# Performance work log

Measured on AMD Instinct MI355X. Metric: run time of the kernel, lower is better.

The kernel has to match this reference:

```python
import jax, jax.numpy as jnp
import numpy as np

B, A = 65536, 32          # batch, n_agents
D, H1, H2, L = 4, 32, 32, 16  # local MLP dims
G_IN, G_H, G_OUT = 2 * L, 32, 2  # global MLP dims


def _lin_init(k, fan_in, fan_out):
    kw, kb = jax.random.split(k)
    s = 1.0 / np.sqrt(fan_in)
    W = jax.random.uniform(kw, (fan_in, fan_out), minval=-s, maxval=s, dtype=jnp.float32)
    b = jax.random.uniform(kb, (fan_out,), minval=-s, maxval=s, dtype=jnp.float32)
    return W, b


def setup_inputs() -> dict:
    key = jax.random.key(0)
    ks = jax.random.split(key, 9)
    x = jax.random.uniform(ks[0], (B, A * D), dtype=jnp.float32)
    oW1, ob1 = _lin_init(ks[1], D, H1)
    oW2, ob2 = _lin_init(ks[2], H1, H2)
    oW3, ob3 = _lin_init(ks[3], H2, L)
    sW1, sb1 = _lin_init(ks[4], D, H1)
    sW2, sb2 = _lin_init(ks[5], H1, H2)
    sW3, sb3 = _lin_init(ks[6], H2, L)
    gW1, gb1 = _lin_init(ks[7], G_IN, G_H)
    gW2, gb2 = _lin_init(ks[8], G_H, G_OUT)
    return {
        "joint_state_actions": x,
        "selected_agent_idx": 5,
        "oW1": oW1, "ob1": ob1, "oW2": oW2, "ob2": ob2, "oW3": oW3, "ob3": ob3,
        "sW1": sW1, "sb1": sb1, "sW2": sW2, "sb2": sb2, "sW3": sW3, "sb3": sb3,
        "gW1": gW1, "gb1": gb1, "gW2": gW2, "gb2": gb2,
    }


def _mlp3(x, W1, b1, W2, b2, W3, b3):
    h = jax.nn.relu(x @ W1 + b1)
    h = jax.nn.relu(h @ W2 + b2)
    return jax.nn.relu(h @ W3 + b3)


def reference(joint_state_actions, selected_agent_idx,
              oW1, ob1, oW2, ob2, oW3, ob3,
              sW1, sb1, sW2, sb2, sW3, sb3,
              gW1, gb1, gW2, gb2):
    xa = joint_state_actions.reshape(-1, A, D)  # [B, A, 4]
    # other-agents stack applied to all agents at once, masked sum over non-selected
    other = _mlp3(xa, oW1, ob1, oW2, ob2, oW3, ob3)  # [B, A, 16]
    mask = (jnp.arange(A) != selected_agent_idx).astype(other.dtype)[None, :, None]
    sum_other = jnp.sum(other * mask, axis=1)  # [B, 16]
    sel_in = xa[:, selected_agent_idx]  # [B, 4] (static index)
    sel_out = _mlp3(sel_in, sW1, sb1, sW2, sb2, sW3, sb3)  # [B, 16]
    h = jax.nn.relu(jnp.concatenate([sel_out, sum_other], axis=1) @ gW1 + gb1)
    q = h @ gW2 + gb2  # [B, 2]
    actions = sel_in[:, 3].astype(jnp.int32)[:, None]  # [B, 1]
    return jnp.take_along_axis(q, actions, axis=1)  # [B, 1]
```

## Files before the change

kernel.cpp:

```cpp
#include <hip/hip_runtime.h>
#include <hip/hip_bf16.h>

#define DEV __device__ __forceinline__

typedef __attribute__((ext_vector_type(8)))  __bf16    bf16x8;
typedef __attribute__((ext_vector_type(4)))  int       int4v;
typedef __attribute__((ext_vector_type(2)))  unsigned  uint2v;
typedef __attribute__((ext_vector_type(16))) float     vfloat16;

#if __has_builtin(__builtin_amdgcn_permlane32_swap)
#define HAVE_PLSWAP 1
#endif

DEV int pkbf(float a, float b) {
    unsigned ua = __builtin_bit_cast(unsigned, a) + 0x8000u;
    unsigned ub = __builtin_bit_cast(unsigned, b) + 0x8000u;
    return (int)__builtin_amdgcn_perm(ua, ub, 0x03020706u);
}

DEV bf16x8 i4_to_frag(int4v v) { return __builtin_bit_cast(bf16x8, v); }

DEV vfloat16 mfma32(bf16x8 a, bf16x8 b, vfloat16 c) {
    return __builtin_amdgcn_mfma_f32_32x32x16_bf16(a, b, c, 0, 0, 0);
}

DEV bf16x8 xposeB(float c0, float c1, float c2, float c3,
                  float c4, float c5, float c6, float c7, bool h) {
    int R0 = pkbf(fmaxf(c0, 0.f), fmaxf(c1, 0.f));
    int R1 = pkbf(fmaxf(c2, 0.f), fmaxf(c3, 0.f));
    int R2 = pkbf(fmaxf(c4, 0.f), fmaxf(c5, 0.f));
    int R3 = pkbf(fmaxf(c6, 0.f), fmaxf(c7, 0.f));
#ifdef HAVE_PLSWAP
    uint2v p0 = __builtin_amdgcn_permlane32_swap((unsigned)R0, (unsigned)R2, false, false);
    uint2v p1 = __builtin_amdgcn_permlane32_swap((unsigned)R1, (unsigned)R3, false, false);
    int4v v;
    v.x = (int)p0.x; v.y = (int)p1.x; v.z = (int)p0.y; v.w = (int)p1.y;
#else
    int S0 = h ? R0 : R2;
    int S1 = h ? R1 : R3;
    int Y0 = __shfl_xor(S0, 32, 64);
    int Y1 = __shfl_xor(S1, 32, 64);
    int4v v;
    v.x = h ? Y0 : R0;
    v.y = h ? Y1 : R1;
    v.z = h ? R2 : Y0;
    v.w = h ? R3 : Y1;
#endif
    return i4_to_frag(v);
}

DEV bf16x8 make_afrag(const float* __restrict__ W, const float* __restrict__ bias,
                      int ld, int Mact, int K, int koff, int lane) {
    int m = lane & 31;
    int h = lane >> 5;
    int d[4];
#pragma unroll
    for (int i = 0; i < 4; ++i) {
        int k0 = koff + h * 8 + 2 * i;
        int k1 = k0 + 1;
        float w0 = 0.f, w1 = 0.f;
        if (m < Mact) {
            if (k0 < K) w0 = W[k0 * ld + m];
            else if (bias && k0 == K) w0 = bias[m];
            if (k1 < K) w1 = W[k1 * ld + m];
            else if (bias && k1 == K) w1 = bias[m];
        }
        d[i] = pkbf(w0, w1);
    }
    int4v v; v.x = d[0]; v.y = d[1]; v.z = d[2]; v.w = d[3];
    return i4_to_frag(v);
}

DEV vfloat16 bvec32(const float* __restrict__ b, int lane) {
    int h = lane >> 5;
    vfloat16 v;
#pragma unroll
    for (int reg = 0; reg < 16; ++reg)
        v[reg] = b[(reg & 3) + 8 * (reg >> 2) + 4 * h];
    return v;
}
DEV vfloat16 bvec16(const float* __restrict__ b, int lane) {
    int h = lane >> 5;
    vfloat16 v;
#pragma unroll
    for (int reg = 0; reg < 16; ++reg)
        v[reg] = (reg < 8) ? b[(reg & 3) + 8 * (reg >> 2) + 4 * h] : 0.f;
    return v;
}

DEV vfloat16 zero16() {
    vfloat16 z;
#pragma unroll
    for (int i = 0; i < 16; ++i) z[i] = 0.f;
    return z;
}

DEV bf16x8 b1_from(int2 d) {
    int4v v;
    v.x = d.x;
    v.y = d.y;
    v.z = 0x00003f80;
    v.w = 0;
    return i4_to_frag(v);
}

struct Frags {
    bf16x8 A1, A2lo, A2hi, A3lo, A3hi;
    vfloat16 b2, b3;
};

DEV void load_frags(Frags& F,
                    const float* __restrict__ W1, const float* __restrict__ b1,
                    const float* __restrict__ W2, const float* __restrict__ b2,
                    const float* __restrict__ W3, const float* __restrict__ b3,
                    int lane) {
    F.A1   = make_afrag(W1, b1,      32, 32, 4,  0,  lane);
    F.A2lo = make_afrag(W2, nullptr, 32, 32, 32, 0,  lane);
    F.A2hi = make_afrag(W2, nullptr, 32, 32, 32, 16, lane);
    F.A3lo = make_afrag(W3, nullptr, 16, 16, 32, 0,  lane);
    F.A3hi = make_afrag(W3, nullptr, 16, 16, 32, 16, lane);
    F.b2 = bvec32(b2, lane);
    F.b3 = bvec16(b3, lane);
}

DEV vfloat16 run_mlp3(bf16x8 B1, const Frags& F, bool h) {
    vfloat16 C1 = mfma32(F.A1, B1, zero16());
    bf16x8 Blo = xposeB(C1[0], C1[1], C1[2], C1[3], C1[4], C1[5], C1[6], C1[7], h);
    bf16x8 Bhi = xposeB(C1[8], C1[9], C1[10], C1[11], C1[12], C1[13], C1[14], C1[15], h);
    vfloat16 C2 = mfma32(F.A2lo, Blo, F.b2);
    C2 = mfma32(F.A2hi, Bhi, C2);
    Blo = xposeB(C2[0], C2[1], C2[2], C2[3], C2[4], C2[5], C2[6], C2[7], h);
    Bhi = xposeB(C2[8], C2[9], C2[10], C2[11], C2[12], C2[13], C2[14], C2[15], h);
    vfloat16 C3 = mfma32(F.A3lo, Blo, F.b3);
    C3 = mfma32(F.A3hi, Bhi, C3);
    return C3;
}

#define XSTRIDE 66

__global__ __launch_bounds__(256)
void dqn_kernel(const float* __restrict__ x, const int* __restrict__ selp,
                const float* __restrict__ oW1, const float* __restrict__ ob1,
                const float* __restrict__ oW2, const float* __restrict__ ob2,
                const float* __restrict__ oW3, const float* __restrict__ ob3,
                const float* __restrict__ sW1, const float* __restrict__ sb1,
                const float* __restrict__ sW2, const float* __restrict__ sb2,
                const float* __restrict__ sW3, const float* __restrict__ sb3,
                const float* __restrict__ gW1, const float* __restrict__ gb1,
                const float* __restrict__ gW2, const float* __restrict__ gb2,
                float* __restrict__ out)
{
    __shared__ int   lds_xb[32 * XSTRIDE];
    __shared__ float lds_red[3][8][64];

    const int tid  = threadIdx.x;
    const int lane = tid & 63;
    const int wave = tid >> 6;
    const bool h = lane >= 32;
    const int c = lane & 31;
    const int sel = *selp;
    const int base0 = blockIdx.x * 32;

    {
        const float* xblk = x + (size_t)base0 * 128;
#pragma unroll
        for (int k = 0; k < 4; ++k) {
            int f = tid + 256 * k;
            int row = f >> 5;
            int ag  = f & 31;
            float4 v = *(const float4*)(xblk + (size_t)f * 4);
            int2 d;
            d.x = pkbf(v.x, v.y);
            d.y = pkbf(v.z, v.w);
            *(int2*)&lds_xb[ag * XSTRIDE + row * 2] = d;
        }
    }

    Frags Fo;
    load_frags(Fo, oW1, ob1, oW2, ob2, oW3, ob3, lane);

    __syncthreads();

    float sum[8] = {0.f, 0.f, 0.f, 0.f, 0.f, 0.f, 0.f, 0.f};
    const int a0 = wave * 8;
    const int* xb = &lds_xb[a0 * XSTRIDE + c * 2];

#pragma unroll
    for (int i = 0; i < 8; i += 2) {
        int2 da = *(const int2*)(xb + i * XSTRIDE);
        int2 db = *(const int2*)(xb + (i + 1) * XSTRIDE);

        vfloat16 C1a = mfma32(Fo.A1, b1_from(da), zero16());
        vfloat16 C1b = mfma32(Fo.A1, b1_from(db), zero16());

        bf16x8 Bal = xposeB(C1a[0], C1a[1], C1a[2], C1a[3], C1a[4], C1a[5], C1a[6], C1a[7], h);
        bf16x8 Bbl = xposeB(C1b[0], C1b[1], C1b[2], C1b[3], C1b[4], C1b[5], C1b[6], C1b[7], h);
        bf16x8 Bah = xposeB(C1a[8], C1a[9], C1a[10], C1a[11], C1a[12], C1a[13], C1a[14], C1a[15], h);
        bf16x8 Bbh = xposeB(C1b[8], C1b[9], C1b[10], C1b[11], C1b[12], C1b[13], C1b[14], C1b[15], h);

        vfloat16 C2a = mfma32(Fo.A2lo, Bal, Fo.b2);
        vfloat16 C2b = mfma32(Fo.A2lo, Bbl, Fo.b2);
        C2a = mfma32(Fo.A2hi, Bah, C2a);
        C2b = mfma32(Fo.A2hi, Bbh, C2b);

        Bal = xposeB(C2a[0], C2a[1], C2a[2], C2a[3], C2a[4], C2a[5], C2a[6], C2a[7], h);
        Bbl = xposeB(C2b[0], C2b[1], C2b[2], C2b[3], C2b[4], C2b[5], C2b[6], C2b[7], h);
        Bah = xposeB(C2a[8], C2a[9], C2a[10], C2a[11], C2a[12], C2a[13], C2a[14], C2a[15], h);
        Bbh = xposeB(C2b[8], C2b[9], C2b[10], C2b[11], C2b[12], C2b[13], C2b[14], C2b[15], h);

        vfloat16 C3a = mfma32(Fo.A3lo, Bal, Fo.b3);
        vfloat16 C3b = mfma32(Fo.A3lo, Bbl, Fo.b3);
        C3a = mfma32(Fo.A3hi, Bah, C3a);
        C3b = mfma32(Fo.A3hi, Bbh, C3b);

        if (a0 + i != sel) {
#pragma unroll
            for (int j = 0; j < 8; ++j) sum[j] += fmaxf(C3a[j], 0.f);
        }
        if (a0 + i + 1 != sel) {
#pragma unroll
            for (int j = 0; j < 8; ++j) sum[j] += fmaxf(C3b[j], 0.f);
        }
    }

    if (wave != 0) {
#pragma unroll
        for (int i = 0; i < 8; ++i) lds_red[wave - 1][i][lane] = sum[i];
    }
    __syncthreads();

    if (wave == 0) {
#pragma unroll
        for (int j = 0; j < 3; ++j)
#pragma unroll
            for (int i = 0; i < 8; ++i) sum[i] += lds_red[j][i][lane];

        Frags Fs;
        load_frags(Fs, sW1, sb1, sW2, sb2, sW3, sb3, lane);
        int2 ds = *(const int2*)&lds_xb[sel * XSTRIDE + c * 2];
        vfloat16 C3s = run_mlp3(b1_from(ds), Fs, h);

        bf16x8 Ag_lo = make_afrag(gW1, nullptr, 32, 32, 32, 0,  lane);
        bf16x8 Ag_hi = make_afrag(gW1, nullptr, 32, 32, 32, 16, lane);
        vfloat16 gb1v = bvec32(gb1, lane);
        bf16x8 Bg_lo = xposeB(C3s[0], C3s[1], C3s[2], C3s[3],
                              C3s[4], C3s[5], C3s[6], C3s[7], h);
        bf16x8 Bg_hi = xposeB(sum[0], sum[1], sum[2], sum[3],
                              sum[4], sum[5], sum[6], sum[7], h);
        vfloat16 G = mfma32(Ag_lo, Bg_lo, gb1v);
        G = mfma32(Ag_hi, Bg_hi, G);
#pragma unroll
        for (int i = 0; i < 16; ++i) G[i] = fmaxf(G[i], 0.f);

        float q0 = 0.f, q1 = 0.f;
#pragma unroll
        for (int reg = 0; reg < 16; ++reg) {
            int row = (reg & 3) + 8 * (reg >> 2) + (h ? 4 : 0);
            q0 += G[reg] * gW2[row * 2 + 0];
            q1 += G[reg] * gW2[row * 2 + 1];
        }
        q0 += __shfl_xor(q0, 32, 64);
        q1 += __shfl_xor(q1, 32, 64);
        q0 += gb2[0];
        q1 += gb2[1];

        if (!h) {
            float f3 = x[(size_t)(base0 + c) * 128 + sel * 4 + 3];
            int act = (int)f3;
            act = act < 0 ? 0 : (act > 1 ? 1 : act);
            out[base0 + c] = act ? q1 : q0;
        }
    }
}

extern "C" void kernel_launch(void* const* d_in, const int* in_sizes, int n_in,
                              void* d_out, int out_size, void* d_ws, size_t ws_size,
                              hipStream_t stream) {
    const float* x   = (const float*)d_in[0];
    const int*   sel = (const int*)d_in[1];
    const float* oW1 = (const float*)d_in[2];
    const float* ob1 = (const float*)d_in[3];
    const float* oW2 = (const float*)d_in[4];
    const float* ob2 = (const float*)d_in[5];
    const float* oW3 = (const float*)d_in[6];
    const float* ob3 = (const float*)d_in[7];
    const float* sW1 = (const float*)d_in[8];
    const float* sb1 = (const float*)d_in[9];
    const float* sW2 = (const float*)d_in[10];
    const float* sb2 = (const float*)d_in[11];
    const float* sW3 = (const float*)d_in[12];
    const float* sb3 = (const float*)d_in[13];
    const float* gW1 = (const float*)d_in[14];
    const float* gb1 = (const float*)d_in[15];
    const float* gW2 = (const float*)d_in[16];
    const float* gb2 = (const float*)d_in[17];
    float* out = (float*)d_out;

    const int B = in_sizes[0] / 128;
    const int blocks = B / 32;
    dqn_kernel<<<blocks, 256, 0, stream>>>(x, sel,
                                           oW1, ob1, oW2, ob2, oW3, ob3,
                                           sW1, sb1, sW2, sb2, sW3, sb3,
                                           gW1, gb1, gW2, gb2, out);
}
```

Measured before the change: 135.2 us.

## Process two batch tiles per block with double-buffered LDS prefetch

Each block now handles two 32-row tiles and uses a double-buffered LDS staging area. Waves 1-3 load and convert the next tile while wave 0 runs the selected-agent and global MLP tail for the current tile. The agent loop processes one agent per iteration instead of two interleaved, adds the layer-3 bias after the MFMA, and pins occupancy with a waves_per_eu attribute. The aim is to hide the serial wave-0 tail and the global-load latency, at the cost of less MFMA interleaving, weights being re-read every tile, and half as many blocks.

```diff
diff --git a/kernel.cpp b/kernel.cpp
--- a/kernel.cpp
+++ b/kernel.cpp
@@ -22,6 +22,13 @@
 
 DEV vfloat16 mfma32(bf16x8 a, bf16x8 b, vfloat16 c) {
     return __builtin_amdgcn_mfma_f32_32x32x16_bf16(a, b, c, 0, 0, 0);
+}
+
+DEV vfloat16 zc() {
+    vfloat16 z;
+#pragma unroll
+    for (int i = 0; i < 16; ++i) z[i] = 0.f;
+    return z;
 }
 
 DEV bf16x8 xposeB(float c0, float c1, float c2, float c3,
@@ -79,21 +86,6 @@
         v[reg] = b[(reg & 3) + 8 * (reg >> 2) + 4 * h];
     return v;
 }
-DEV vfloat16 bvec16(const float* __restrict__ b, int lane) {
-    int h = lane >> 5;
-    vfloat16 v;
-#pragma unroll
-    for (int reg = 0; reg < 16; ++reg)
-        v[reg] = (reg < 8) ? b[(reg & 3) + 8 * (reg >> 2) + 4 * h] : 0.f;
-    return v;
-}
-
-DEV vfloat16 zero16() {
-    vfloat16 z;
-#pragma unroll
-    for (int i = 0; i < 16; ++i) z[i] = 0.f;
-    return z;
-}
 
 DEV bf16x8 b1_from(int2 d) {
     int4v v;
@@ -104,41 +96,11 @@
     return i4_to_frag(v);
 }
 
-struct Frags {
-    bf16x8 A1, A2lo, A2hi, A3lo, A3hi;
-    vfloat16 b2, b3;
-};
-
-DEV void load_frags(Frags& F,
-                    const float* __restrict__ W1, const float* __restrict__ b1,
-                    const float* __restrict__ W2, const float* __restrict__ b2,
-                    const float* __restrict__ W3, const float* __restrict__ b3,
-                    int lane) {
-    F.A1   = make_afrag(W1, b1,      32, 32, 4,  0,  lane);
-    F.A2lo = make_afrag(W2, nullptr, 32, 32, 32, 0,  lane);
-    F.A2hi = make_afrag(W2, nullptr, 32, 32, 32, 16, lane);
-    F.A3lo = make_afrag(W3, nullptr, 16, 16, 32, 0,  lane);
-    F.A3hi = make_afrag(W3, nullptr, 16, 16, 32, 16, lane);
-    F.b2 = bvec32(b2, lane);
-    F.b3 = bvec16(b3, lane);
-}
-
-DEV vfloat16 run_mlp3(bf16x8 B1, const Frags& F, bool h) {
-    vfloat16 C1 = mfma32(F.A1, B1, zero16());
-    bf16x8 Blo = xposeB(C1[0], C1[1], C1[2], C1[3], C1[4], C1[5], C1[6], C1[7], h);
-    bf16x8 Bhi = xposeB(C1[8], C1[9], C1[10], C1[11], C1[12], C1[13], C1[14], C1[15], h);
-    vfloat16 C2 = mfma32(F.A2lo, Blo, F.b2);
-    C2 = mfma32(F.A2hi, Bhi, C2);
-    Blo = xposeB(C2[0], C2[1], C2[2], C2[3], C2[4], C2[5], C2[6], C2[7], h);
-    Bhi = xposeB(C2[8], C2[9], C2[10], C2[11], C2[12], C2[13], C2[14], C2[15], h);
-    vfloat16 C3 = mfma32(F.A3lo, Blo, F.b3);
-    C3 = mfma32(F.A3hi, Bhi, C3);
-    return C3;
-}
-
 #define XSTRIDE 66
+#define TILES_PER_BLK 2
 
 __global__ __launch_bounds__(256)
+__attribute__((amdgpu_waves_per_eu(4, 4)))
 void dqn_kernel(const float* __restrict__ x, const int* __restrict__ selp,
                 const float* __restrict__ oW1, const float* __restrict__ ob1,
                 const float* __restrict__ oW2, const float* __restrict__ ob2,
@@ -150,7 +112,7 @@
                 const float* __restrict__ gW2, const float* __restrict__ gb2,
                 float* __restrict__ out)
 {
-    __shared__ int   lds_xb[32 * XSTRIDE];
+    __shared__ int   lds_xb[2][32 * XSTRIDE];
     __shared__ float lds_red[3][8][64];
 
     const int tid  = threadIdx.x;
@@ -159,10 +121,10 @@
     const bool h = lane >= 32;
     const int c = lane & 31;
     const int sel = *selp;
-    const int base0 = blockIdx.x * 32;
 
     {
-        const float* xblk = x + (size_t)base0 * 128;
+        int tile0 = blockIdx.x * TILES_PER_BLK;
+        const float* xblk = x + (size_t)tile0 * 32 * 128;
 #pragma unroll
         for (int k = 0; k < 4; ++k) {
             int f = tid + 256 * k;
@@ -172,103 +134,127 @@
             int2 d;
             d.x = pkbf(v.x, v.y);
             d.y = pkbf(v.z, v.w);
-            *(int2*)&lds_xb[ag * XSTRIDE + row * 2] = d;
+            *(int2*)&lds_xb[0][ag * XSTRIDE + row * 2] = d;
         }
     }
 
-    Frags Fo;
-    load_frags(Fo, oW1, ob1, oW2, ob2, oW3, ob3, lane);
-
-    __syncthreads();
-
-    float sum[8] = {0.f, 0.f, 0.f, 0.f, 0.f, 0.f, 0.f, 0.f};
-    const int a0 = wave * 8;
-    const int* xb = &lds_xb[a0 * XSTRIDE + c * 2];
-
-#pragma unroll
-    for (int i = 0; i < 8; i += 2) {
-        int2 da = *(const int2*)(xb + i * XSTRIDE);
-        int2 db = *(const int2*)(xb + (i + 1) * XSTRIDE);
-
-        vfloat16 C1a = mfma32(Fo.A1, b1_from(da), zero16());
-        vfloat16 C1b = mfma32(Fo.A1, b1_from(db), zero16());
-
-        bf16x8 Bal = xposeB(C1a[0], C1a[1], C1a[2], C1a[3], C1a[4], C1a[5], C1a[6], C1a[7], h);
-        bf16x8 Bbl = xposeB(C1b[0], C1b[1], C1b[2], C1b[3], C1b[4], C1b[5], C1b[6], C1b[7], h);
-        bf16x8 Bah = xposeB(C1a[8], C1a[9], C1a[10], C1a[11], C1a[12], C1a[13], C1a[14], C1a[15], h);
-        bf16x8 Bbh = xposeB(C1b[8], C1b[9], C1b[10], C1b[11], C1b[12], C1b[13], C1b[14], C1b[15], h);
-
-        vfloat16 C2a = mfma32(Fo.A2lo, Bal, Fo.b2);
-        vfloat16 C2b = mfma32(Fo.A2lo, Bbl, Fo.b2);
-        C2a = mfma32(Fo.A2hi, Bah, C2a);
-        C2b = mfma32(Fo.A2hi, Bbh, C2b);
-
-        Bal = xposeB(C2a[0], C2a[1], C2a[2], C2a[3], C2a[4], C2a[5], C2a[6], C2a[7], h);
-        Bbl = xposeB(C2b[0], C2b[1], C2b[2], C2b[3], C2b[4], C2b[5], C2b[6], C2b[7], h);
-        Bah = xposeB(C2a[8], C2a[9], C2a[10], C2a[11], C2a[12], C2a[13], C2a[14], C2a[15], h);
-        Bbh = xposeB(C2b[8], C2b[9], C2b[10], C2b[11], C2b[12], C2b[13], C2b[14], C2b[15], h);
-
-        vfloat16 C3a = mfma32(Fo.A3lo, Bal, Fo.b3);
-        vfloat16 C3b = mfma32(Fo.A3lo, Bbl, Fo.b3);
-        C3a = mfma32(Fo.A3hi, Bah, C3a);
-        C3b = mfma32(Fo.A3hi, Bbh, C3b);
-
-        if (a0 + i != sel) {
-#pragma unroll
-            for (int j = 0; j < 8; ++j) sum[j] += fmaxf(C3a[j], 0.f);
-        }
-        if (a0 + i + 1 != sel) {
-#pragma unroll
-            for (int j = 0; j < 8; ++j) sum[j] += fmaxf(C3b[j], 0.f);
-        }
-    }
-
-    if (wave != 0) {
-#pragma unroll
-        for (int i = 0; i < 8; ++i) lds_red[wave - 1][i][lane] = sum[i];
-    }
-    __syncthreads();
-
-    if (wave == 0) {
-#pragma unroll
-        for (int j = 0; j < 3; ++j)
-#pragma unroll
-            for (int i = 0; i < 8; ++i) sum[i] += lds_red[j][i][lane];
-
-        Frags Fs;
-        load_frags(Fs, sW1, sb1, sW2, sb2, sW3, sb3, lane);
-        int2 ds = *(const int2*)&lds_xb[sel * XSTRIDE + c * 2];
-        vfloat16 C3s = run_mlp3(b1_from(ds), Fs, h);
-
-        bf16x8 Ag_lo = make_afrag(gW1, nullptr, 32, 32, 32, 0,  lane);
-        bf16x8 Ag_hi = make_afrag(gW1, nullptr, 32, 32, 32, 16, lane);
-        vfloat16 gb1v = bvec32(gb1, lane);
-        bf16x8 Bg_lo = xposeB(C3s[0], C3s[1], C3s[2], C3s[3],
-                              C3s[4], C3s[5], C3s[6], C3s[7], h);
-        bf16x8 Bg_hi = xposeB(sum[0], sum[1], sum[2], sum[3],
-                              sum[4], sum[5], sum[6], sum[7], h);
-        vfloat16 G = mfma32(Ag_lo, Bg_lo, gb1v);
-        G = mfma32(Ag_hi, Bg_hi, G);
-#pragma unroll
-        for (int i = 0; i < 16; ++i) G[i] = fmaxf(G[i], 0.f);
-
-        float q0 = 0.f, q1 = 0.f;
-#pragma unroll
-        for (int reg = 0; reg < 16; ++reg) {
-            int row = (reg & 3) + 8 * (reg >> 2) + (h ? 4 : 0);
-            q0 += G[reg] * gW2[row * 2 + 0];
-            q1 += G[reg] * gW2[row * 2 + 1];
-        }
-        q0 += __shfl_xor(q0, 32, 64);
-        q1 += __shfl_xor(q1, 32, 64);
-        q0 += gb2[0];
-        q1 += gb2[1];
-
-        if (!h) {
-            float f3 = x[(size_t)(base0 + c) * 128 + sel * 4 + 3];
-            int act = (int)f3;
-            act = act < 0 ? 0 : (act > 1 ? 1 : act);
-            out[base0 + c] = act ? q1 : q0;
+    for (int t = 0; t < TILES_PER_BLK; ++t) {
+        const int tile  = blockIdx.x * TILES_PER_BLK + t;
+        const int base0 = tile * 32;
+        const int buf   = t & 1;
+
+        bf16x8 A1   = make_afrag(oW1, ob1,     32, 32, 4,  0,  lane);
+        bf16x8 A2lo = make_afrag(oW2, nullptr, 32, 32, 32, 0,  lane);
+        bf16x8 A2hi = make_afrag(oW2, nullptr, 32, 32, 32, 16, lane);
+        bf16x8 A3lo = make_afrag(oW3, nullptr, 16, 16, 32, 0,  lane);
+        bf16x8 A3hi = make_afrag(oW3, nullptr, 16, 16, 32, 16, lane);
+        vfloat16 b2 = bvec32(ob2, lane);
+        float b3s[8];
+#pragma unroll
+        for (int j = 0; j < 8; ++j) b3s[j] = ob3[(j & 3) + 8 * (j >> 2) + (h ? 4 : 0)];
+
+        __syncthreads();
+
+        float sum[8] = {0.f, 0.f, 0.f, 0.f, 0.f, 0.f, 0.f, 0.f};
+        const int a0 = wave * 8;
+        const int* xb = &lds_xb[buf][a0 * XSTRIDE + c * 2];
+
+#pragma unroll
+        for (int i = 0; i < 8; ++i) {
+            int2 da = *(const int2*)(xb + i * XSTRIDE);
+            vfloat16 C1 = mfma32(A1, b1_from(da), zc());
+            bf16x8 Blo = xposeB(C1[0], C1[1], C1[2], C1[3], C1[4], C1[5], C1[6], C1[7], h);
+            bf16x8 Bhi = xposeB(C1[8], C1[9], C1[10], C1[11], C1[12], C1[13], C1[14], C1[15], h);
+            vfloat16 C2 = mfma32(A2lo, Blo, b2);
+            C2 = mfma32(A2hi, Bhi, C2);
+            Blo = xposeB(C2[0], C2[1], C2[2], C2[3], C2[4], C2[5], C2[6], C2[7], h);
+            Bhi = xposeB(C2[8], C2[9], C2[10], C2[11], C2[12], C2[13], C2[14], C2[15], h);
+            vfloat16 C3 = mfma32(A3lo, Blo, zc());
+            C3 = mfma32(A3hi, Bhi, C3);
+            if (a0 + i != sel) {
+#pragma unroll
+                for (int j = 0; j < 8; ++j) sum[j] += fmaxf(C3[j] + b3s[j], 0.f);
+            }
+        }
+
+        if (wave != 0) {
+#pragma unroll
+            for (int i = 0; i < 8; ++i) lds_red[wave - 1][i][lane] = sum[i];
+        }
+        __syncthreads();
+
+        if (wave != 0) {
+            if (t + 1 < TILES_PER_BLK) {
+                const float* xblk = x + (size_t)(base0 + 32) * 128;
+                for (int f = tid - 64; f < 1024; f += 192) {
+                    int row = f >> 5;
+                    int ag  = f & 31;
+                    float4 v = *(const float4*)(xblk + (size_t)f * 4);
+                    int2 d;
+                    d.x = pkbf(v.x, v.y);
+                    d.y = pkbf(v.z, v.w);
+                    *(int2*)&lds_xb[buf ^ 1][ag * XSTRIDE + row * 2] = d;
+                }
+            }
+        } else {
+#pragma unroll
+            for (int j = 0; j < 3; ++j)
+#pragma unroll
+                for (int i = 0; i < 8; ++i) sum[i] += lds_red[j][i][lane];
+
+            bf16x8 S1   = make_afrag(sW1, sb1,     32, 32, 4,  0,  lane);
+            bf16x8 S2lo = make_afrag(sW2, nullptr, 32, 32, 32, 0,  lane);
+            bf16x8 S2hi = make_afrag(sW2, nullptr, 32, 32, 32, 16, lane);
+            bf16x8 S3lo = make_afrag(sW3, nullptr, 16, 16, 32, 0,  lane);
+            bf16x8 S3hi = make_afrag(sW3, nullptr, 16, 16, 32, 16, lane);
+            vfloat16 sb2v = bvec32(sb2, lane);
+            float sb3s[8];
+#pragma unroll
+            for (int j = 0; j < 8; ++j) sb3s[j] = sb3[(j & 3) + 8 * (j >> 2) + (h ? 4 : 0)];
+
+            int2 dsx = *(const int2*)&lds_xb[buf][sel * XSTRIDE + c * 2];
+            vfloat16 C1 = mfma32(S1, b1_from(dsx), zc());
+            bf16x8 Blo = xposeB(C1[0], C1[1], C1[2], C1[3], C1[4], C1[5], C1[6], C1[7], h);
+            bf16x8 Bhi = xposeB(C1[8], C1[9], C1[10], C1[11], C1[12], C1[13], C1[14], C1[15], h);
+            vfloat16 C2 = mfma32(S2lo, Blo, sb2v);
+            C2 = mfma32(S2hi, Bhi, C2);
+            Blo = xposeB(C2[0], C2[1], C2[2], C2[3], C2[4], C2[5], C2[6], C2[7], h);
+            Bhi = xposeB(C2[8], C2[9], C2[10], C2[11], C2[12], C2[13], C2[14], C2[15], h);
+            vfloat16 C3s = mfma32(S3lo, Blo, zc());
+            C3s = mfma32(S3hi, Bhi, C3s);
+
+            bf16x8 Ag_lo = make_afrag(gW1, nullptr, 32, 32, 32, 0,  lane);
+            bf16x8 Ag_hi = make_afrag(gW1, nullptr, 32, 32, 32, 16, lane);
+            vfloat16 gb1v = bvec32(gb1, lane);
+            bf16x8 Bg_lo = xposeB(C3s[0] + sb3s[0], C3s[1] + sb3s[1],
+                                  C3s[2] + sb3s[2], C3s[3] + sb3s[3],
+                                  C3s[4] + sb3s[4], C3s[5] + sb3s[5],
+                                  C3s[6] + sb3s[6], C3s[7] + sb3s[7], h);
+            bf16x8 Bg_hi = xposeB(sum[0], sum[1], sum[2], sum[3],
+                                  sum[4], sum[5], sum[6], sum[7], h);
+            vfloat16 G = mfma32(Ag_lo, Bg_lo, gb1v);
+            G = mfma32(Ag_hi, Bg_hi, G);
+#pragma unroll
+            for (int i = 0; i < 16; ++i) G[i] = fmaxf(G[i], 0.f);
+
+            float q0 = 0.f, q1 = 0.f;
+#pragma unroll
+            for (int reg = 0; reg < 16; ++reg) {
+                int row = (reg & 3) + 8 * (reg >> 2) + (h ? 4 : 0);
+                q0 += G[reg] * gW2[row * 2 + 0];
+                q1 += G[reg] * gW2[row * 2 + 1];
+            }
+            q0 += __shfl_xor(q0, 32, 64);
+            q1 += __shfl_xor(q1, 32, 64);
+            q0 += gb2[0];
+            q1 += gb2[1];
+
+            if (!h) {
+                float f3 = x[(size_t)(base0 + c) * 128 + sel * 4 + 3];
+                int act = (int)f3;
+                act = act < 0 ? 0 : (act > 1 ? 1 : act);
+                out[base0 + c] = act ? q1 : q0;
+            }
         }
     }
 }
@@ -297,7 +283,7 @@
     float* out = (float*)d_out;
 
     const int B = in_sizes[0] / 128;
-    const int blocks = B / 32;
+    const int blocks = B / (32 * TILES_PER_BLK);
     dqn_kernel<<<blocks, 256, 0, stream>>>(x, sel,
                                            oW1, ob1, oW2, ob2, oW3, ob3,
                                            sW1, sb1, sW2, sb2, sW3, sb3,
```

Result: slower. 209.7 us (+55.2%).

## Give each wave its own 32-row batch tile and drop block barriers

Applied to the files above, without the earlier changes.

Each wave now owns a full 32-row batch tile and loops over all 32 agents, where before four waves split the agents of one tile. This removes both __syncthreads, the LDS cross-wave reduction, and the serial tail in which only wave 0 ran the selected-agent and global MLPs. The action value is also captured in LDS during the load instead of being reread from global memory. In exchange each block handles four times more rows, so there are four times fewer blocks. LDS use per block grows, and the agent loop is no longer unrolled.

```diff
diff --git a/kernel.cpp b/kernel.cpp
--- a/kernel.cpp
+++ b/kernel.cpp
@@ -150,8 +150,8 @@
                 const float* __restrict__ gW2, const float* __restrict__ gb2,
                 float* __restrict__ out)
 {
-    __shared__ int   lds_xb[32 * XSTRIDE];
-    __shared__ float lds_red[3][8][64];
+    __shared__ int   lds_xb[4][32 * XSTRIDE];
+    __shared__ float lds_act[4][32];
 
     const int tid  = threadIdx.x;
     const int lane = tid & 63;
@@ -159,34 +159,31 @@
     const bool h = lane >= 32;
     const int c = lane & 31;
     const int sel = *selp;
-    const int base0 = blockIdx.x * 32;
+    const int base0 = blockIdx.x * 128 + wave * 32;
 
     {
         const float* xblk = x + (size_t)base0 * 128;
 #pragma unroll
-        for (int k = 0; k < 4; ++k) {
-            int f = tid + 256 * k;
+        for (int k = 0; k < 16; ++k) {
+            int f = lane + 64 * k;
             int row = f >> 5;
             int ag  = f & 31;
             float4 v = *(const float4*)(xblk + (size_t)f * 4);
+            if (ag == sel) lds_act[wave][row] = v.w;
             int2 d;
             d.x = pkbf(v.x, v.y);
             d.y = pkbf(v.z, v.w);
-            *(int2*)&lds_xb[ag * XSTRIDE + row * 2] = d;
+            *(int2*)&lds_xb[wave][ag * XSTRIDE + row * 2] = d;
         }
     }
 
     Frags Fo;
     load_frags(Fo, oW1, ob1, oW2, ob2, oW3, ob3, lane);
 
-    __syncthreads();
-
     float sum[8] = {0.f, 0.f, 0.f, 0.f, 0.f, 0.f, 0.f, 0.f};
-    const int a0 = wave * 8;
-    const int* xb = &lds_xb[a0 * XSTRIDE + c * 2];
-
-#pragma unroll
-    for (int i = 0; i < 8; i += 2) {
+    const int* xb = &lds_xb[wave][c * 2];
+
+    for (int i = 0; i < 32; i += 2) {
         int2 da = *(const int2*)(xb + i * XSTRIDE);
         int2 db = *(const int2*)(xb + (i + 1) * XSTRIDE);
 
@@ -213,63 +210,50 @@
         C3a = mfma32(Fo.A3hi, Bah, C3a);
         C3b = mfma32(Fo.A3hi, Bbh, C3b);
 
-        if (a0 + i != sel) {
+        if (i != sel) {
 #pragma unroll
             for (int j = 0; j < 8; ++j) sum[j] += fmaxf(C3a[j], 0.f);
         }
-        if (a0 + i + 1 != sel) {
+        if (i + 1 != sel) {
 #pragma unroll
             for (int j = 0; j < 8; ++j) sum[j] += fmaxf(C3b[j], 0.f);
         }
     }
 
-    if (wave != 0) {
-#pragma unroll
-        for (int i = 0; i < 8; ++i) lds_red[wave - 1][i][lane] = sum[i];
-    }
-    __syncthreads();
-
-    if (wave == 0) {
-#pragma unroll
-        for (int j = 0; j < 3; ++j)
-#pragma unroll
-            for (int i = 0; i < 8; ++i) sum[i] += lds_red[j][i][lane];
-
-        Frags Fs;
-        load_frags(Fs, sW1, sb1, sW2, sb2, sW3, sb3, lane);
-        int2 ds = *(const int2*)&lds_xb[sel * XSTRIDE + c * 2];
-        vfloat16 C3s = run_mlp3(b1_from(ds), Fs, h);
-
-        bf16x8 Ag_lo = make_afrag(gW1, nullptr, 32, 32, 32, 0,  lane);
-        bf16x8 Ag_hi = make_afrag(gW1, nullptr, 32, 32, 32, 16, lane);
-        vfloat16 gb1v = bvec32(gb1, lane);
-        bf16x8 Bg_lo = xposeB(C3s[0], C3s[1], C3s[2], C3s[3],
-                              C3s[4], C3s[5], C3s[6], C3s[7], h);
-        bf16x8 Bg_hi = xposeB(sum[0], sum[1], sum[2], sum[3],
-                              sum[4], sum[5], sum[6], sum[7], h);
-        vfloat16 G = mfma32(Ag_lo, Bg_lo, gb1v);
-        G = mfma32(Ag_hi, Bg_hi, G);
-#pragma unroll
-        for (int i = 0; i < 16; ++i) G[i] = fmaxf(G[i], 0.f);
-
-        float q0 = 0.f, q1 = 0.f;
-#pragma unroll
-        for (int reg = 0; reg < 16; ++reg) {
-            int row = (reg & 3) + 8 * (reg >> 2) + (h ? 4 : 0);
-            q0 += G[reg] * gW2[row * 2 + 0];
-            q1 += G[reg] * gW2[row * 2 + 1];
-        }
-        q0 += __shfl_xor(q0, 32, 64);
-        q1 += __shfl_xor(q1, 32, 64);
-        q0 += gb2[0];
-        q1 += gb2[1];
-
-        if (!h) {
-            float f3 = x[(size_t)(base0 + c) * 128 + sel * 4 + 3];
-            int act = (int)f3;
-            act = act < 0 ? 0 : (act > 1 ? 1 : act);
-            out[base0 + c] = act ? q1 : q0;
-        }
+    Frags Fs;
+    load_frags(Fs, sW1, sb1, sW2, sb2, sW3, sb3, lane);
+    int2 dsx = *(const int2*)&lds_xb[wave][sel * XSTRIDE + c * 2];
+    vfloat16 C3s = run_mlp3(b1_from(dsx), Fs, h);
+
+    bf16x8 Ag_lo = make_afrag(gW1, nullptr, 32, 32, 32, 0,  lane);
+    bf16x8 Ag_hi = make_afrag(gW1, nullptr, 32, 32, 32, 16, lane);
+    vfloat16 gb1v = bvec32(gb1, lane);
+    bf16x8 Bg_lo = xposeB(C3s[0], C3s[1], C3s[2], C3s[3],
+                          C3s[4], C3s[5], C3s[6], C3s[7], h);
+    bf16x8 Bg_hi = xposeB(sum[0], sum[1], sum[2], sum[3],
+                          sum[4], sum[5], sum[6], sum[7], h);
+    vfloat16 G = mfma32(Ag_lo, Bg_lo, gb1v);
+    G = mfma32(Ag_hi, Bg_hi, G);
+#pragma unroll
+    for (int i = 0; i < 16; ++i) G[i] = fmaxf(G[i], 0.f);
+
+    float q0 = 0.f, q1 = 0.f;
+#pragma unroll
+    for (int reg = 0; reg < 16; ++reg) {
+        int row = (reg & 3) + 8 * (reg >> 2) + (h ? 4 : 0);
+        q0 += G[reg] * gW2[row * 2 + 0];
+        q1 += G[reg] * gW2[row * 2 + 1];
+    }
+    q0 += __shfl_xor(q0, 32, 64);
+    q1 += __shfl_xor(q1, 32, 64);
+    q0 += gb2[0];
+    q1 += gb2[1];
+
+    if (!h) {
+        float f3 = lds_act[wave][c];
+        int act = (int)f3;
+        act = act < 0 ? 0 : (act > 1 ? 1 : act);
+        out[base0 + c] = act ? q1 : q0;
     }
 }
 
@@ -297,7 +281,7 @@
     float* out = (float*)d_out;
 
     const int B = in_sizes[0] / 128;
-    const int blocks = B / 32;
+    const int blocks = B / 128;
     dqn_kernel<<<blocks, 256, 0, stream>>>(x, sel,
                                            oW1, ob1, oW2, ob2, oW3, ob3,
                                            sW1, sb1, sW2, sb2, sW3, sb3,
```

After: 137.3 us. No clear change (+1.6%).
